# Kernel tuning notes

Hardware: AMD Instinct MI355X
Metric: run time of the kernel (lower is better)

Reference implementation:

```python
import jax, jax.numpy as jnp
import numpy as np

INPUT_SIZE = 256
HIDDEN_SIZE = 512
OUTPUT_SIZE = 512
BATCH = 32
SEQ_LEN = 1024


def _linear(x, W, b):
    # torch nn.Linear: y = x @ W.T + b, W: [out, in]
    return x @ W.T + b


def _cell(x, h, c, Wf, bf, Wi, bi, Wc, bc, Wo, bo):
    combined = jnp.concatenate([x, h], axis=1)
    f = jax.nn.sigmoid(_linear(combined, Wf, bf))
    i = jax.nn.sigmoid(_linear(combined, Wi, bi))
    g = jnp.tanh(_linear(combined, Wc, bc))
    o = jax.nn.sigmoid(_linear(combined, Wo, bo))
    c_new = f * c + i * g
    h_new = o * jnp.tanh(c_new)
    return h_new, c_new


def setup_inputs() -> dict:
    key = jax.random.key(0)
    ks = jax.random.split(key, 17)
    d = {"x": jax.random.normal(ks[0], (BATCH, SEQ_LEN, INPUT_SIZE), dtype=jnp.float32)}
    # layer 0: input_size -> hidden_size; layer 1: hidden_size -> output_size
    specs = [(0, INPUT_SIZE, HIDDEN_SIZE), (1, HIDDEN_SIZE, OUTPUT_SIZE)]
    ki = 1
    for layer, in_sz, out_sz in specs:
        for gate in ("f", "i", "c", "o"):
            d[f"W{layer}_{gate}"] = jax.random.normal(ks[ki], (out_sz, in_sz + out_sz), dtype=jnp.float32) * 0.02
            d[f"b{layer}_{gate}"] = jnp.zeros((out_sz,), dtype=jnp.float32)
            ki += 1
    return d


def reference(x, W0_f, b0_f, W0_i, b0_i, W0_c, b0_c, W0_o, b0_o,
              W1_f, b1_f, W1_i, b1_i, W1_c, b1_c, W1_o, b1_o):
    B = x.shape[0]
    h0 = jnp.zeros((B, HIDDEN_SIZE), dtype=x.dtype)
    c0 = jnp.zeros((B, HIDDEN_SIZE), dtype=x.dtype)
    h1 = jnp.zeros((B, OUTPUT_SIZE), dtype=x.dtype)
    c1 = jnp.zeros((B, OUTPUT_SIZE), dtype=x.dtype)

    def step(carry, x_t):
        h0, c0, h1, c1 = carry
        h0, c0 = _cell(x_t, h0, c0, W0_f, b0_f, W0_i, b0_i, W0_c, b0_c, W0_o, b0_o)
        h1, c1 = _cell(h0, h1, c1, W1_f, b1_f, W1_i, b1_i, W1_c, b1_c, W1_o, b1_o)
        return (h0, c0, h1, c1), h1

    xs = jnp.swapaxes(x, 0, 1)  # [seq, batch, feat]
    _, ys = jax.lax.scan(step, (h0, c0, h1, c1), xs)
    return jnp.swapaxes(ys, 0, 1)  # stack along dim=1: [batch, seq, out]
```

## Files before the change

### kernel.cpp

```cpp
#include <hip/hip_runtime.h>
#include <stdint.h>


#define SEQ   1024
#define NB    32
#define HID   512
#define NWG   64
#define L0WGS 32
#define FSTRIDE 16
#define SPIN_BUDGET (1 << 20)
#define ROWB  1040
#define SMEM_MISC 11776
#define SMEM_BYTES (SMEM_MISC + 3 * 32 * ROWB)

typedef __attribute__((ext_vector_type(8))) short s16x8;
typedef __attribute__((ext_vector_type(4))) float f32x4;

__device__ __forceinline__ uint16_t f2bf(float x) {
    uint32_t u = __float_as_uint(x);
    return (uint16_t)((u + 0x7FFFu + ((u >> 16) & 1u)) >> 16);
}
__device__ __forceinline__ uint32_t pack2bf(float a, float b) {
    return (uint32_t)f2bf(a) | ((uint32_t)f2bf(b) << 16);
}
__device__ __forceinline__ s16x8 pack8(const float* p) {
    float4 a = *(const float4*)p;
    float4 b = *(const float4*)(p + 4);
    s16x8 r;
    r[0] = (short)f2bf(a.x); r[1] = (short)f2bf(a.y);
    r[2] = (short)f2bf(a.z); r[3] = (short)f2bf(a.w);
    r[4] = (short)f2bf(b.x); r[5] = (short)f2bf(b.y);
    r[6] = (short)f2bf(b.z); r[7] = (short)f2bf(b.w);
    return r;
}
__device__ __forceinline__ f32x4 mfma16(s16x8 a, s16x8 b, f32x4 c) {
    return __builtin_amdgcn_mfma_f32_16x16x32_bf16(a, b, c, 0, 0, 0);
}
__device__ __forceinline__ float sigm(float x) { return 1.0f / (1.0f + __expf(-x)); }
__device__ __forceinline__ float tanh_(float x) { return 1.0f - 2.0f / (__expf(2.0f * x) + 1.0f); }

__device__ __forceinline__ void st_u32(uint32_t* p, uint32_t v) {
    __hip_atomic_store(p, v, __ATOMIC_RELAXED, __HIP_MEMORY_SCOPE_AGENT);
}
__device__ __forceinline__ void st_u64(uint64_t* p, uint64_t v) {
    __hip_atomic_store(p, v, __ATOMIC_RELAXED, __HIP_MEMORY_SCOPE_AGENT);
}
__device__ __forceinline__ void st_u8(uint8_t* p, uint8_t v) {
    __hip_atomic_store(p, v, __ATOMIC_RELAXED, __HIP_MEMORY_SCOPE_AGENT);
}
__device__ __forceinline__ unsigned ld_flag(const unsigned* p) {
    return __hip_atomic_load(p, __ATOMIC_RELAXED, __HIP_MEMORY_SCOPE_AGENT);
}
__device__ __forceinline__ void poll_all32(const unsigned* p, int& budget) {
    const int lane = threadIdx.x & 63;
    for (;;) {
        bool ok = (lane >= 8) || (ld_flag(p + lane) == 0x01010101u);
        if (__all(ok)) break;
        if (--budget < 0) break;
        __builtin_amdgcn_s_sleep(1);
    }
    asm volatile("" ::: "memory");
}

__device__ __forceinline__ void dma16(const void* g, void* l) {
    __builtin_amdgcn_global_load_lds(
        (const __attribute__((address_space(1))) unsigned int*)g,
        (__attribute__((address_space(3))) unsigned int*)l, 16, 0, 0);
}
__device__ __forceinline__ void stage32(const char* gbase, size_t gstride,
                                        char* lbase, int lane, int wv) {
#pragma unroll
    for (int i = 0; i < 8; ++i) {
        const int r = wv * 8 + i;
        dma16(gbase + (size_t)r * gstride + (size_t)lane * 16, lbase + r * ROWB);
    }
}

struct Shared {
    float gbuf[4][NB][18];
    float cbuf[NB][18];
    float bbuf[4][16];
};

__device__ __forceinline__ void load_bias_c(Shared& sh,
        const float* bf_, const float* bi_, const float* bc_, const float* bo_,
        int col0) {
    const int tid = threadIdx.x;
    if (tid < 16)       sh.bbuf[0][tid]      = bf_[col0 + tid];
    else if (tid < 32)  sh.bbuf[1][tid - 16] = bi_[col0 + tid - 16];
    else if (tid < 48)  sh.bbuf[2][tid - 32] = bc_[col0 + tid - 32];
    else if (tid < 64)  sh.bbuf[3][tid - 48] = bo_[col0 + tid - 48];
    float2 z = make_float2(0.f, 0.f);
    ((float2*)sh.cbuf)[tid] = z;
    if (tid < 32) ((float2*)sh.cbuf)[256 + tid] = z;
}

__device__ __forceinline__ float2 gates2(Shared& sh, int b, int n) {
    float2 pf = *(float2*)&sh.gbuf[0][b][n];
    float2 pi = *(float2*)&sh.gbuf[1][b][n];
    float2 pc = *(float2*)&sh.gbuf[2][b][n];
    float2 po = *(float2*)&sh.gbuf[3][b][n];
    float2 h;
    {
        float f = sigm(pf.x + sh.bbuf[0][n]);
        float i = sigm(pi.x + sh.bbuf[1][n]);
        float g = tanh_(pc.x + sh.bbuf[2][n]);
        float o = sigm(po.x + sh.bbuf[3][n]);
        float c = f * sh.cbuf[b][n] + i * g;
        sh.cbuf[b][n] = c;
        h.x = o * tanh_(c);
    }
    {
        float f = sigm(pf.y + sh.bbuf[0][n + 1]);
        float i = sigm(pi.y + sh.bbuf[1][n + 1]);
        float g = tanh_(pc.y + sh.bbuf[2][n + 1]);
        float o = sigm(po.y + sh.bbuf[3][n + 1]);
        float c = f * sh.cbuf[b][n + 1] + i * g;
        sh.cbuf[b][n + 1] = c;
        h.y = o * tanh_(c);
    }
    return h;
}

extern __shared__ char smem[];

__device__ void body_l0(const float* __restrict__ xg,
                        const float* __restrict__ Wf, const float* __restrict__ Wi,
                        const float* __restrict__ Wc, const float* __restrict__ Wo,
                        const float* __restrict__ bf_, const float* __restrict__ bi_,
                        const float* __restrict__ bc_, const float* __restrict__ bo_,
                        uint16_t* __restrict__ ring0, unsigned* __restrict__ flags0,
                        int w)
{
    const int tid  = threadIdx.x;
    const int wave = tid >> 6;
    const int lane = tid & 63;
    const int nloc = lane & 15;
    const int quad = lane >> 4;
    const int col0 = w * 16;
    int budget = SPIN_BUDGET;

    Shared& sh = *(Shared*)smem;
    char* hbuf  = smem + SMEM_MISC;
    char* xbufA = hbuf + 32 * ROWB;
    char* xbufB = xbufA + 32 * ROWB;
    load_bias_c(sh, bf_, bi_, bc_, bo_, col0);

    const float* Wg = (wave == 0) ? Wf : (wave == 1) ? Wi : (wave == 2) ? Wc : Wo;
    const float* wrow = Wg + (size_t)(col0 + nloc) * 768 + quad * 8;
    s16x8 B[24];
#pragma unroll
    for (int kt = 0; kt < 24; ++kt) B[kt] = pack8(wrow + kt * 32);

    uint32_t* ring0w = (uint32_t*)ring0;

    stage32((const char*)xg,        (size_t)SEQ * 1024, xbufA, lane, wave);
    stage32((const char*)xg + 1024, (size_t)SEQ * 1024, xbufB, lane, wave);
    __builtin_amdgcn_s_waitcnt(0);
    __syncthreads();
    f32x4 xa0 = {0.f, 0.f, 0.f, 0.f};
    f32x4 xa1 = {0.f, 0.f, 0.f, 0.f};
    {
        const char* pxl  = xbufA + nloc * ROWB + quad * 32;
        const char* pxl2 = pxl + 16 * ROWB;
#pragma unroll
        for (int kt = 0; kt < 8; ++kt) {
            xa0 = mfma16(pack8((const float*)(pxl  + kt * 128)), B[kt], xa0);
            xa1 = mfma16(pack8((const float*)(pxl2 + kt * 128)), B[kt], xa1);
        }
    }

#pragma unroll 1
    for (int t = 0; t < SEQ; ++t) {
        if (t > 0) {
            poll_all32(&flags0[(size_t)(t - 1) * FSTRIDE], budget);
            stage32((const char*)ring0 + (size_t)(t - 1) * 32768, 1024,
                    hbuf, lane, wave);
        }
        __builtin_amdgcn_s_waitcnt(0);
        __syncthreads();

        f32x4 acc0 = xa0;
        f32x4 acc1 = xa1;
        if (t > 0) {
            const char* ph  = hbuf + nloc * ROWB + quad * 16;
            const char* ph2 = ph + 16 * ROWB;
#pragma unroll
            for (int kt = 0; kt < 16; ++kt) {
                acc0 = mfma16(*(const s16x8*)(ph  + kt * 64), B[8 + kt], acc0);
                acc1 = mfma16(*(const s16x8*)(ph2 + kt * 64), B[8 + kt], acc1);
            }
        }
#pragma unroll
        for (int r = 0; r < 4; ++r) {
            sh.gbuf[wave][quad * 4 + r][nloc]      = acc0[r];
            sh.gbuf[wave][16 + quad * 4 + r][nloc] = acc1[r];
        }
        __syncthreads();
        {
            const int b = tid >> 3, n = (tid & 7) * 2;
            float2 h = gates2(sh, b, n);
            st_u32(ring0w + ((size_t)t * NB + b) * (HID / 2) + (col0 + n) / 2,
                   pack2bf(h.x, h.y));
        }
        __syncthreads();
        if (tid == 0)
            st_u8((uint8_t*)&flags0[(size_t)t * FSTRIDE] + w, 1);

        if (t + 1 < SEQ) {
            const char* xb = ((t + 1) & 1) ? xbufB : xbufA;
            const char* pxl  = xb + nloc * ROWB + quad * 32;
            const char* pxl2 = pxl + 16 * ROWB;
            f32x4 a0 = {0.f, 0.f, 0.f, 0.f};
            f32x4 a1 = {0.f, 0.f, 0.f, 0.f};
#pragma unroll
            for (int kt = 0; kt < 8; ++kt) {
                a0 = mfma16(pack8((const float*)(pxl  + kt * 128)), B[kt], a0);
                a1 = mfma16(pack8((const float*)(pxl2 + kt * 128)), B[kt], a1);
            }
            xa0 = a0; xa1 = a1;
        }
        if (t + 2 < SEQ)
            stage32((const char*)xg + (size_t)(t + 2) * 1024, (size_t)SEQ * 1024,
                    (t & 1) ? xbufB : xbufA, lane, wave);
    }
}

template<bool R1>
__device__ void body_l1(const float* __restrict__ Wf, const float* __restrict__ Wi,
                        const float* __restrict__ Wc, const float* __restrict__ Wo,
                        const float* __restrict__ bf_, const float* __restrict__ bi_,
                        const float* __restrict__ bc_, const float* __restrict__ bo_,
                        float* __restrict__ out,
                        uint16_t* __restrict__ ring0, uint16_t* __restrict__ ring1,
                        unsigned* __restrict__ flags0, unsigned* __restrict__ flags1,
                        int w)
{
    const int tid  = threadIdx.x;
    const int wave = tid >> 6;
    const int lane = tid & 63;
    const int nloc = lane & 15;
    const int quad = lane >> 4;
    const int col0 = w * 16;
    int budget = SPIN_BUDGET;

    Shared& sh = *(Shared*)smem;
    char* hbuf0 = smem + SMEM_MISC;
    char* hbuf1 = hbuf0 + 32 * ROWB;
    load_bias_c(sh, bf_, bi_, bc_, bo_, col0);

    const float* Wg = (wave == 0) ? Wf : (wave == 1) ? Wi : (wave == 2) ? Wc : Wo;
    const float* wrow = Wg + (size_t)(col0 + nloc) * 1024 + quad * 8;
    s16x8 B[32];
#pragma unroll
    for (int kt = 0; kt < 32; ++kt) B[kt] = pack8(wrow + kt * 32);

    uint32_t* ring1w = (uint32_t*)ring1;
    __syncthreads();

    poll_all32(&flags0[0], budget);
    stage32((const char*)ring0, 1024, hbuf0, lane, wave);

#pragma unroll 1
    for (int t = 0; t < SEQ; ++t) {
        if (t > 0) {
            poll_all32(&flags1[(size_t)(t - 1) * FSTRIDE], budget);
            if (R1)
                stage32((const char*)ring1 + (size_t)(t - 1) * 32768, 1024,
                        hbuf1, lane, wave);
        }
        __builtin_amdgcn_s_waitcnt(0);
        __syncthreads();

        f32x4 acc0 = {0.f, 0.f, 0.f, 0.f};
        f32x4 acc1 = {0.f, 0.f, 0.f, 0.f};
        {
            const char* ph  = hbuf0 + nloc * ROWB + quad * 16;
            const char* ph2 = ph + 16 * ROWB;
#pragma unroll
            for (int kt = 0; kt < 16; ++kt) {
                acc0 = mfma16(*(const s16x8*)(ph  + kt * 64), B[kt], acc0);
                acc1 = mfma16(*(const s16x8*)(ph2 + kt * 64), B[kt], acc1);
            }
        }
        if (t > 0) {
            if (R1) {
                const char* ph  = hbuf1 + nloc * ROWB + quad * 16;
                const char* ph2 = ph + 16 * ROWB;
#pragma unroll
                for (int kt = 0; kt < 16; ++kt) {
                    acc0 = mfma16(*(const s16x8*)(ph  + kt * 64), B[16 + kt], acc0);
                    acc1 = mfma16(*(const s16x8*)(ph2 + kt * 64), B[16 + kt], acc1);
                }
            } else {
                const float* po0 = out + ((size_t)nloc * SEQ + (t - 1)) * HID + quad * 8;
                const float* po1 = po0 + (size_t)16 * SEQ * HID;
#pragma unroll
                for (int kt = 0; kt < 16; ++kt) {
                    acc0 = mfma16(pack8(po0 + kt * 32), B[16 + kt], acc0);
                    acc1 = mfma16(pack8(po1 + kt * 32), B[16 + kt], acc1);
                }
            }
        }
#pragma unroll
        for (int r = 0; r < 4; ++r) {
            sh.gbuf[wave][quad * 4 + r][nloc]      = acc0[r];
            sh.gbuf[wave][16 + quad * 4 + r][nloc] = acc1[r];
        }
        __syncthreads();
        {
            const int b = tid >> 3, n = (tid & 7) * 2;
            float2 h = gates2(sh, b, n);
            float* po = &out[((size_t)b * SEQ + t) * HID + col0 + n];
            if (R1) {
                *(float2*)po = h;
                st_u32(ring1w + ((size_t)t * NB + b) * (HID / 2) + (col0 + n) / 2,
                       pack2bf(h.x, h.y));
            } else {
                uint64_t v = (uint64_t)__float_as_uint(h.x)
                           | ((uint64_t)__float_as_uint(h.y) << 32);
                st_u64((uint64_t*)po, v);
            }
        }
        __syncthreads();
        if (tid == 0)
            st_u8((uint8_t*)&flags1[(size_t)t * FSTRIDE] + w, 1);

        if (t + 1 < SEQ) {
            poll_all32(&flags0[(size_t)(t + 1) * FSTRIDE], budget);
            stage32((const char*)ring0 + (size_t)(t + 1) * 32768, 1024,
                    hbuf0, lane, wave);
        }
    }
}

template<bool R1>
__global__ __launch_bounds__(256, 1) void lstm_k(
    const float* __restrict__ x,
    const float* W0f, const float* b0f, const float* W0i, const float* b0i,
    const float* W0c, const float* b0c, const float* W0o, const float* b0o,
    const float* W1f, const float* b1f, const float* W1i, const float* b1i,
    const float* W1c, const float* b1c, const float* W1o, const float* b1o,
    float* out, uint16_t* ring0, uint16_t* ring1,
    unsigned* flags0, unsigned* flags1)
{
    if (blockIdx.x < L0WGS)
        body_l0(x, W0f, W0i, W0c, W0o, b0f, b0i, b0c, b0o,
                ring0, flags0, blockIdx.x);
    else
        body_l1<R1>(W1f, W1i, W1c, W1o, b1f, b1i, b1c, b1o,
                    out, ring0, ring1, flags0, flags1, blockIdx.x - L0WGS);
}

extern "C" void kernel_launch(void* const* d_in, const int* in_sizes, int n_in,
                              void* d_out, int out_size, void* d_ws, size_t ws_size,
                              hipStream_t stream) {
    const float* x   = (const float*)d_in[0];
    const float* W0f = (const float*)d_in[1];  const float* b0f = (const float*)d_in[2];
    const float* W0i = (const float*)d_in[3];  const float* b0i = (const float*)d_in[4];
    const float* W0c = (const float*)d_in[5];  const float* b0c = (const float*)d_in[6];
    const float* W0o = (const float*)d_in[7];  const float* b0o = (const float*)d_in[8];
    const float* W1f = (const float*)d_in[9];  const float* b1f = (const float*)d_in[10];
    const float* W1i = (const float*)d_in[11]; const float* b1i = (const float*)d_in[12];
    const float* W1c = (const float*)d_in[13]; const float* b1c = (const float*)d_in[14];
    const float* W1o = (const float*)d_in[15]; const float* b1o = (const float*)d_in[16];
    float* out = (float*)d_out;

    const size_t flag_bytes = (size_t)SEQ * FSTRIDE * 4;
    const size_t ring_bytes = (size_t)SEQ * NB * HID * 2;
    unsigned* flags0 = (unsigned*)d_ws;
    unsigned* flags1 = flags0 + SEQ * FSTRIDE;
    uint16_t* ring0  = (uint16_t*)((char*)d_ws + 2 * flag_bytes);
    uint16_t* ring1  = (uint16_t*)((char*)d_ws + 2 * flag_bytes + ring_bytes);
    const bool use_r1 = ws_size >= 2 * flag_bytes + 2 * ring_bytes;

    hipFuncSetAttribute((const void*)lstm_k<true>,
                        hipFuncAttributeMaxDynamicSharedMemorySize, SMEM_BYTES);
    hipFuncSetAttribute((const void*)lstm_k<false>,
                        hipFuncAttributeMaxDynamicSharedMemorySize, SMEM_BYTES);

    hipMemsetAsync(d_ws, 0, 2 * flag_bytes, stream);

    if (use_r1)
        hipLaunchKernelGGL(lstm_k<true>, dim3(NWG), dim3(256), SMEM_BYTES, stream,
            x, W0f, b0f, W0i, b0i, W0c, b0c, W0o, b0o,
            W1f, b1f, W1i, b1i, W1c, b1c, W1o, b1o,
            out, ring0, ring1, flags0, flags1);
    else
        hipLaunchKernelGGL(lstm_k<false>, dim3(NWG), dim3(256), SMEM_BYTES, stream,
            x, W0f, b0f, W0i, b0i, W0c, b0c, W0o, b0o,
            W1f, b1f, W1i, b1i, W1c, b1c, W1o, b1o,
            out, ring0, ring1, flags0, flags1);
}
```

Before: 4.068 ms.

## Halve workgroup count by giving each workgroup 32 columns with 8 waves

Each layer now runs on 16 workgroups of 512 threads instead of 32 of 256, and each workgroup computes 32 hidden columns, two 16-column halves per gate. Flag polling drops to 16 byte-flags per step and each wave stages fewer rows of the hidden-state ring. The aim is to cut cross-workgroup synchronisation fan-in and the redundant per-step reloads of the shared hidden state. The cost is fewer CUs in use and more waves sharing one CU's LDS bandwidth and barriers.

```diff
diff --git a/kernel.cpp b/kernel.cpp
--- a/kernel.cpp
+++ b/kernel.cpp
@@ -5,12 +5,13 @@
 #define SEQ   1024
 #define NB    32
 #define HID   512
-#define NWG   64
-#define L0WGS 32
+#define NWG   32
+#define LWGS  16
+#define COLS  32
 #define FSTRIDE 16
 #define SPIN_BUDGET (1 << 20)
 #define ROWB  1040
-#define SMEM_MISC 11776
+#define SMEM_MISC 22272
 #define SMEM_BYTES (SMEM_MISC + 3 * 32 * ROWB)
 
 typedef __attribute__((ext_vector_type(8))) short s16x8;
@@ -51,10 +52,10 @@
 __device__ __forceinline__ unsigned ld_flag(const unsigned* p) {
     return __hip_atomic_load(p, __ATOMIC_RELAXED, __HIP_MEMORY_SCOPE_AGENT);
 }
-__device__ __forceinline__ void poll_all32(const unsigned* p, int& budget) {
+__device__ __forceinline__ void poll16(const unsigned* p, int& budget) {
     const int lane = threadIdx.x & 63;
     for (;;) {
-        bool ok = (lane >= 8) || (ld_flag(p + lane) == 0x01010101u);
+        bool ok = (lane >= 4) || (ld_flag(p + lane) == 0x01010101u);
         if (__all(ok)) break;
         if (--budget < 0) break;
         __builtin_amdgcn_s_sleep(1);
@@ -70,29 +71,29 @@
 __device__ __forceinline__ void stage32(const char* gbase, size_t gstride,
                                         char* lbase, int lane, int wv) {
 #pragma unroll
-    for (int i = 0; i < 8; ++i) {
-        const int r = wv * 8 + i;
+    for (int i = 0; i < 4; ++i) {
+        const int r = wv * 4 + i;
         dma16(gbase + (size_t)r * gstride + (size_t)lane * 16, lbase + r * ROWB);
     }
 }
 
 struct Shared {
-    float gbuf[4][NB][18];
-    float cbuf[NB][18];
-    float bbuf[4][16];
+    float gbuf[4][NB][34];
+    float cbuf[NB][34];
+    float bbuf[4][COLS];
 };
 
 __device__ __forceinline__ void load_bias_c(Shared& sh,
         const float* bf_, const float* bi_, const float* bc_, const float* bo_,
-        int col0) {
+        int colw) {
     const int tid = threadIdx.x;
-    if (tid < 16)       sh.bbuf[0][tid]      = bf_[col0 + tid];
-    else if (tid < 32)  sh.bbuf[1][tid - 16] = bi_[col0 + tid - 16];
-    else if (tid < 48)  sh.bbuf[2][tid - 32] = bc_[col0 + tid - 32];
-    else if (tid < 64)  sh.bbuf[3][tid - 48] = bo_[col0 + tid - 48];
+    if (tid < 32)        sh.bbuf[0][tid]       = bf_[colw + tid];
+    else if (tid < 64)   sh.bbuf[1][tid - 32]  = bi_[colw + tid - 32];
+    else if (tid < 96)   sh.bbuf[2][tid - 64]  = bc_[colw + tid - 64];
+    else if (tid < 128)  sh.bbuf[3][tid - 96]  = bo_[colw + tid - 96];
     float2 z = make_float2(0.f, 0.f);
     ((float2*)sh.cbuf)[tid] = z;
-    if (tid < 32) ((float2*)sh.cbuf)[256 + tid] = z;
+    if (tid < 32) ((float2*)sh.cbuf)[512 + tid] = z;
 }
 
 __device__ __forceinline__ float2 gates2(Shared& sh, int b, int n) {
@@ -137,17 +138,20 @@
     const int lane = tid & 63;
     const int nloc = lane & 15;
     const int quad = lane >> 4;
-    const int col0 = w * 16;
+    const int gate = wave & 3;
+    const int hh   = wave >> 2;
+    const int colw = w * COLS;
+    const int colv = colw + hh * 16;
     int budget = SPIN_BUDGET;
 
     Shared& sh = *(Shared*)smem;
     char* hbuf  = smem + SMEM_MISC;
     char* xbufA = hbuf + 32 * ROWB;
     char* xbufB = xbufA + 32 * ROWB;
-    load_bias_c(sh, bf_, bi_, bc_, bo_, col0);
-
-    const float* Wg = (wave == 0) ? Wf : (wave == 1) ? Wi : (wave == 2) ? Wc : Wo;
-    const float* wrow = Wg + (size_t)(col0 + nloc) * 768 + quad * 8;
+    load_bias_c(sh, bf_, bi_, bc_, bo_, colw);
+
+    const float* Wg = (gate == 0) ? Wf : (gate == 1) ? Wi : (gate == 2) ? Wc : Wo;
+    const float* wrow = Wg + (size_t)(colv + nloc) * 768 + quad * 8;
     s16x8 B[24];
 #pragma unroll
     for (int kt = 0; kt < 24; ++kt) B[kt] = pack8(wrow + kt * 32);
@@ -173,7 +177,7 @@
 #pragma unroll 1
     for (int t = 0; t < SEQ; ++t) {
         if (t > 0) {
-            poll_all32(&flags0[(size_t)(t - 1) * FSTRIDE], budget);
+            poll16(&flags0[(size_t)(t - 1) * FSTRIDE], budget);
             stage32((const char*)ring0 + (size_t)(t - 1) * 32768, 1024,
                     hbuf, lane, wave);
         }
@@ -193,14 +197,14 @@
         }
 #pragma unroll
         for (int r = 0; r < 4; ++r) {
-            sh.gbuf[wave][quad * 4 + r][nloc]      = acc0[r];
-            sh.gbuf[wave][16 + quad * 4 + r][nloc] = acc1[r];
+            sh.gbuf[gate][quad * 4 + r][hh * 16 + nloc]      = acc0[r];
+            sh.gbuf[gate][16 + quad * 4 + r][hh * 16 + nloc] = acc1[r];
         }
         __syncthreads();
         {
-            const int b = tid >> 3, n = (tid & 7) * 2;
+            const int b = tid >> 4, n = (tid & 15) * 2;
             float2 h = gates2(sh, b, n);
-            st_u32(ring0w + ((size_t)t * NB + b) * (HID / 2) + (col0 + n) / 2,
+            st_u32(ring0w + ((size_t)t * NB + b) * (HID / 2) + (colw + n) / 2,
                    pack2bf(h.x, h.y));
         }
         __syncthreads();
@@ -241,16 +245,19 @@
     const int lane = tid & 63;
     const int nloc = lane & 15;
     const int quad = lane >> 4;
-    const int col0 = w * 16;
+    const int gate = wave & 3;
+    const int hh   = wave >> 2;
+    const int colw = w * COLS;
+    const int colv = colw + hh * 16;
     int budget = SPIN_BUDGET;
 
     Shared& sh = *(Shared*)smem;
     char* hbuf0 = smem + SMEM_MISC;
     char* hbuf1 = hbuf0 + 32 * ROWB;
-    load_bias_c(sh, bf_, bi_, bc_, bo_, col0);
-
-    const float* Wg = (wave == 0) ? Wf : (wave == 1) ? Wi : (wave == 2) ? Wc : Wo;
-    const float* wrow = Wg + (size_t)(col0 + nloc) * 1024 + quad * 8;
+    load_bias_c(sh, bf_, bi_, bc_, bo_, colw);
+
+    const float* Wg = (gate == 0) ? Wf : (gate == 1) ? Wi : (gate == 2) ? Wc : Wo;
+    const float* wrow = Wg + (size_t)(colv + nloc) * 1024 + quad * 8;
     s16x8 B[32];
 #pragma unroll
     for (int kt = 0; kt < 32; ++kt) B[kt] = pack8(wrow + kt * 32);
@@ -258,13 +265,13 @@
     uint32_t* ring1w = (uint32_t*)ring1;
     __syncthreads();
 
-    poll_all32(&flags0[0], budget);
+    poll16(&flags0[0], budget);
     stage32((const char*)ring0, 1024, hbuf0, lane, wave);
 
 #pragma unroll 1
     for (int t = 0; t < SEQ; ++t) {
         if (t > 0) {
-            poll_all32(&flags1[(size_t)(t - 1) * FSTRIDE], budget);
+            poll16(&flags1[(size_t)(t - 1) * FSTRIDE], budget);
             if (R1)
                 stage32((const char*)ring1 + (size_t)(t - 1) * 32768, 1024,
                         hbuf1, lane, wave);
@@ -304,17 +311,17 @@
         }
 #pragma unroll
         for (int r = 0; r < 4; ++r) {
-            sh.gbuf[wave][quad * 4 + r][nloc]      = acc0[r];
-            sh.gbuf[wave][16 + quad * 4 + r][nloc] = acc1[r];
+            sh.gbuf[gate][quad * 4 + r][hh * 16 + nloc]      = acc0[r];
+            sh.gbuf[gate][16 + quad * 4 + r][hh * 16 + nloc] = acc1[r];
         }
         __syncthreads();
         {
-            const int b = tid >> 3, n = (tid & 7) * 2;
+            const int b = tid >> 4, n = (tid & 15) * 2;
             float2 h = gates2(sh, b, n);
-            float* po = &out[((size_t)b * SEQ + t) * HID + col0 + n];
+            float* po = &out[((size_t)b * SEQ + t) * HID + colw + n];
             if (R1) {
                 *(float2*)po = h;
-                st_u32(ring1w + ((size_t)t * NB + b) * (HID / 2) + (col0 + n) / 2,
+                st_u32(ring1w + ((size_t)t * NB + b) * (HID / 2) + (colw + n) / 2,
                        pack2bf(h.x, h.y));
             } else {
                 uint64_t v = (uint64_t)__float_as_uint(h.x)
@@ -327,7 +334,7 @@
             st_u8((uint8_t*)&flags1[(size_t)t * FSTRIDE] + w, 1);
 
         if (t + 1 < SEQ) {
-            poll_all32(&flags0[(size_t)(t + 1) * FSTRIDE], budget);
+            poll16(&flags0[(size_t)(t + 1) * FSTRIDE], budget);
             stage32((const char*)ring0 + (size_t)(t + 1) * 32768, 1024,
                     hbuf0, lane, wave);
         }
@@ -335,7 +342,7 @@
 }
 
 template<bool R1>
-__global__ __launch_bounds__(256, 1) void lstm_k(
+__global__ __launch_bounds__(512, 2) void lstm_k(
     const float* __restrict__ x,
     const float* W0f, const float* b0f, const float* W0i, const float* b0i,
     const float* W0c, const float* b0c, const float* W0o, const float* b0o,
@@ -344,12 +351,12 @@
     float* out, uint16_t* ring0, uint16_t* ring1,
     unsigned* flags0, unsigned* flags1)
 {
-    if (blockIdx.x < L0WGS)
+    if (blockIdx.x < LWGS)
         body_l0(x, W0f, W0i, W0c, W0o, b0f, b0i, b0c, b0o,
                 ring0, flags0, blockIdx.x);
     else
         body_l1<R1>(W1f, W1i, W1c, W1o, b1f, b1i, b1c, b1o,
-                    out, ring0, ring1, flags0, flags1, blockIdx.x - L0WGS);
+                    out, ring0, ring1, flags0, flags1, blockIdx.x - LWGS);
 }
 
 extern "C" void kernel_launch(void* const* d_in, const int* in_sizes, int n_in,
@@ -382,12 +389,12 @@
     hipMemsetAsync(d_ws, 0, 2 * flag_bytes, stream);
 
     if (use_r1)
-        hipLaunchKernelGGL(lstm_k<true>, dim3(NWG), dim3(256), SMEM_BYTES, stream,
+        hipLaunchKernelGGL(lstm_k<true>, dim3(NWG), dim3(512), SMEM_BYTES, stream,
             x, W0f, b0f, W0i, b0i, W0c, b0c, W0o, b0o,
             W1f, b1f, W1i, b1i, W1c, b1c, W1o, b1o,
             out, ring0, ring1, flags0, flags1);
     else
-        hipLaunchKernelGGL(lstm_k<false>, dim3(NWG), dim3(256), SMEM_BYTES, stream,
+        hipLaunchKernelGGL(lstm_k<false>, dim3(NWG), dim3(512), SMEM_BYTES, stream,
             x, W0f, b0f, W0i, b0i, W0c, b0c, W0o, b0o,
             W1f, b1f, W1i, b1i, W1c, b1c, W1o, b1o,
             out, ring0, ring1, flags0, flags1);
```

Result: slower. 5.072 ms (+24.7%).
